# Kernel tuning notes

Measured on AMD Instinct MI355X. Metric: run time of the kernel, lower is better.

The kernel has to match this reference:

```python
import jax, jax.numpy as jnp
import numpy as np

B, D, L, K = 4096, 1280, 16384, 64


def setup_inputs() -> dict:
    key = jax.random.key(0)
    k1, k2, k3, k4, k5 = jax.random.split(key, 5)
    scale_enc = 1.0 / np.sqrt(D)
    scale_dec = 1.0 / np.sqrt(L)
    return {
        "x_BD": jax.random.normal(k1, (B, D), dtype=jnp.float32),
        "pb_D": jax.random.normal(k2, (D,), dtype=jnp.float32) * 0.01,
        "W_enc": jax.random.normal(k3, (D, L), dtype=jnp.float32) * scale_enc,
        "lb_L": jax.random.normal(k4, (L,), dtype=jnp.float32) * 0.01,
        "W_dec": jax.random.normal(k5, (L, D), dtype=jnp.float32) * scale_dec,
    }


def topk_activation(x_BL, k):
    # lax.top_k over last dim, relu the values, scatter back into zeros
    tv_Bk, ti_Bk = jax.lax.top_k(x_BL, k)
    tv_Bk = jax.nn.relu(tv_Bk)
    b_B = jnp.arange(x_BL.shape[0])[:, None]
    return jnp.zeros_like(x_BL).at[b_B, ti_Bk].set(tv_Bk)


def reference(x_BD, pb_D, W_enc, lb_L, W_dec):
    # encode: shift by pre-bias, dense, add latent bias
    xshift_BD = x_BD - pb_D
    zpre_BL = xshift_BD @ W_enc + lb_L          # [B, L]
    # top-k sparse activation
    z_BL = topk_activation(zpre_BL, K)          # [B, L], only K nonzeros per row
    # decode: dense matmul over full L (the kernel-headroom target)
    xhat_BD = z_BL @ W_dec + pb_D               # [B, D]
    return (zpre_BL, z_BL, xhat_BD)
```

## Files before the change

### kernel.cpp

```cpp
#include <hip/hip_runtime.h>
#include <hip/hip_bf16.h>
#include <stdint.h>

#define B_SZ 4096
#define D_SZ 1280
#define L_SZ 16384
#define K_TOP 64
#define C_CAP 192
#define BAND 0.07f

typedef __attribute__((ext_vector_type(8))) short s16x8;
typedef __attribute__((ext_vector_type(4))) float f32x4;

#define GLOAD_LDS16(gp, lp)                                                          \
  __builtin_amdgcn_global_load_lds((const __attribute__((address_space(1))) void*)(gp), \
                                   (__attribute__((address_space(3))) void*)(lp), 16, 0, 0)

static __device__ __forceinline__ unsigned short f2bf(float f) {
  __hip_bfloat16 h = __float2bfloat16(f);
  return *reinterpret_cast<unsigned short*>(&h);
}
static __device__ __forceinline__ float bf2f(unsigned short u) {
  return __uint_as_float((unsigned)u << 16);
}
static __device__ __forceinline__ unsigned mkkey(float f) {
  const unsigned u = __float_as_uint(f);
  return (u & 0x80000000u) ? ~u : (u | 0x80000000u);
}
static __device__ __forceinline__ float unkey(unsigned k) {
  const unsigned u = (k & 0x80000000u) ? (k & 0x7fffffffu) : ~k;
  return __uint_as_float(u);
}

__global__ __launch_bounds__(256) void sae_prep(const float* __restrict__ x,
                                                const float* __restrict__ pb,
                                                const float* __restrict__ We,
                                                const float* __restrict__ Wd,
                                                unsigned short* __restrict__ A,
                                                float* __restrict__ xs,
                                                float* __restrict__ WT,
                                                unsigned short* __restrict__ WbT,
                                                unsigned short* __restrict__ Wdb,
                                                int* __restrict__ bk_cnt) {
  const int b = blockIdx.x, t = threadIdx.x;
  if (b < 5120) {
    __shared__ float tile[64][65];
    const int l0 = (b & 255) * 64, d0 = (b >> 8) * 64;
    const int c = t & 63, rg = t >> 6;
#pragma unroll
    for (int i = 0; i < 16; ++i) {
      const int row = i * 4 + rg;
      tile[row][c] = We[(size_t)(d0 + row) * L_SZ + l0 + c];
    }
    __syncthreads();
#pragma unroll
    for (int i = 0; i < 16; ++i) {
      const int row = i * 4 + rg;
      const float v = tile[c][row];
      const size_t o = (size_t)(l0 + row) * D_SZ + d0 + c;
      WT[o] = v;
      WbT[o] = f2bf(v);
    }
  } else if (b < 5120 + 4096) {
    const int r = b - 5120;
    const float* xr = x + (size_t)r * D_SZ;
    unsigned short* ar = A + (size_t)r * D_SZ;
    float* sr = xs + (size_t)r * D_SZ;
    for (int d = t; d < D_SZ; d += 256) {
      const float v = xr[d] - pb[d];
      ar[d] = f2bf(v);
      sr[d] = v;
    }
  } else if (b < 5120 + 4096 + 2048) {
    const int n4 = L_SZ * D_SZ / 4;
    for (int i = (b - 9216) * 256 + t; i < n4; i += 2048 * 256) {
      const float4 v = ((const float4*)Wd)[i];
      ushort4 o;
      o.x = f2bf(v.x); o.y = f2bf(v.y); o.z = f2bf(v.z); o.w = f2bf(v.w);
      ((ushort4*)Wdb)[i] = o;
    }
  } else {
    bk_cnt[(b - 11264) * 256 + t] = 0;
  }
}

#define SWZ(lin) ((lin) ^ ((((lin) >> 9) & 7) << 4))
#define A_LDS 0
#define B_LDS 65536
#define KBYTES (D_SZ * 2)

#define PH_MID()                                          \
  __builtin_amdgcn_s_barrier();                           \
  asm volatile("s_waitcnt lgkmcnt(0)" ::: "memory");      \
  __builtin_amdgcn_sched_barrier(0);                      \
  __builtin_amdgcn_s_setprio(1)

#define PH_END()                                          \
  __builtin_amdgcn_s_setprio(0);                          \
  __builtin_amdgcn_s_barrier();                           \
  __builtin_amdgcn_sched_barrier(0)

__global__ __launch_bounds__(512, 2) void sae_gemm(const unsigned short* __restrict__ A,
                                                   const unsigned short* __restrict__ WT,
                                                   const float* __restrict__ lb,
                                                   float* __restrict__ zpre) {
  __shared__ short lds[65536];
  char* ldsc = (char*)lds;
  const int t = threadIdx.x, lane = t & 63, w = t >> 6;
  const int wr = w >> 2, wc = w & 3, w2 = w * 2;

  const int bid = blockIdx.x;
  const int xcd = bid & 7, i2 = bid >> 3;
  const int b2 = i2 >> 4, inner = i2 & 15;
  const int mt = (b2 & 3) * 4 + (inner & 3);
  const int nt = xcd * 8 + (b2 >> 2) * 4 + (inner >> 2);
  const int m0 = mt * 256, n0 = nt * 256;

  f32x4 acc[8][4] = {};

  auto STAGE = [&](const unsigned short* op, int rowbase, int ldsop, int buf, int half, int tile) {
#pragma unroll
    for (int s = 0; s < 2; ++s) {
      const int o = (w2 + s) * 1024 + lane * 16;
      const int r = o >> 7;
      const int cb = (o & 127) ^ (((o >> 9) & 7) << 4);
      const char* g = (const char*)op + (size_t)(rowbase + half * 128 + r) * KBYTES +
                      tile * 128 + cb;
      char* l = ldsc + ldsop + buf * 32768 + half * 16384 + (w2 + s) * 1024;
      GLOAD_LDS16(g, l);
    }
  };
  auto LDA = [&](s16x8* af, int buf, int q) {
#pragma unroll
    for (int i = 0; i < 2; ++i)
#pragma unroll
      for (int kk = 0; kk < 2; ++kk) {
        const int r = (q * 2 + i) * 16 + (lane & 15);
        int lin = r * 128 + kk * 64 + ((lane >> 4) * 16);
        lin = SWZ(lin);
        af[i * 2 + kk] = *(const s16x8*)(ldsc + A_LDS + buf * 32768 + wr * 16384 + lin);
      }
  };
  auto LDB = [&](s16x8* bg, int buf) {
#pragma unroll
    for (int j = 0; j < 4; ++j)
#pragma unroll
      for (int kk = 0; kk < 2; ++kk) {
        const int nloc = wc * 64 + j * 16 + (lane & 15);
        const int half = nloc >> 7, r = nloc & 127;
        int lin = r * 128 + kk * 64 + ((lane >> 4) * 16);
        lin = SWZ(lin);
        bg[j * 2 + kk] = *(const s16x8*)(ldsc + B_LDS + buf * 32768 + half * 16384 + lin);
      }
  };
  auto MM = [&](s16x8* af, s16x8* bg, int q) {
#pragma unroll
    for (int i = 0; i < 2; ++i)
#pragma unroll
      for (int j = 0; j < 4; ++j)
#pragma unroll
        for (int kk = 0; kk < 2; ++kk)
          acc[q * 2 + i][j] =
              __builtin_amdgcn_mfma_f32_16x16x32_bf16(af[i * 2 + kk], bg[j * 2 + kk],
                                                      acc[q * 2 + i][j], 0, 0, 0);
  };

  STAGE(WT, n0, B_LDS, 0, 0, 0); STAGE(WT, n0, B_LDS, 0, 1, 0);
  STAGE(A, m0, A_LDS, 0, 0, 0);  STAGE(A, m0, A_LDS, 0, 1, 0);
  STAGE(WT, n0, B_LDS, 1, 0, 1); STAGE(WT, n0, B_LDS, 1, 1, 1);
  asm volatile("s_waitcnt vmcnt(4)" ::: "memory");
  __builtin_amdgcn_s_barrier();
  __builtin_amdgcn_sched_barrier(0);

  const int NI = D_SZ / 128;
  for (int i = 0; i < NI; ++i) {
    const bool last = (i == NI - 1);
    s16x8 af[4], bg[8];
    LDB(bg, 0); LDA(af, 0, 0);
    STAGE(A, m0, A_LDS, 1, 0, 2 * i + 1); STAGE(A, m0, A_LDS, 1, 1, 2 * i + 1);
    PH_MID(); MM(af, bg, 0); PH_END();
    LDA(af, 0, 1);
    if (!last) STAGE(WT, n0, B_LDS, 0, 0, 2 * i + 2);
    PH_MID(); MM(af, bg, 1); PH_END();
    LDA(af, 0, 2);
    if (!last) STAGE(WT, n0, B_LDS, 0, 1, 2 * i + 2);
    PH_MID(); MM(af, bg, 2); PH_END();
    LDA(af, 0, 3);
    PH_MID(); MM(af, bg, 3);
    __builtin_amdgcn_s_setprio(0);
    if (last) { asm volatile("s_waitcnt vmcnt(0)" ::: "memory"); }
    else      { asm volatile("s_waitcnt vmcnt(4)" ::: "memory"); }
    __builtin_amdgcn_s_barrier();
    __builtin_amdgcn_sched_barrier(0);
    LDB(bg, 1); LDA(af, 1, 0);
    if (!last) STAGE(A, m0, A_LDS, 0, 0, 2 * i + 2);
    PH_MID(); MM(af, bg, 0); PH_END();
    LDA(af, 1, 1);
    if (!last) STAGE(A, m0, A_LDS, 0, 1, 2 * i + 2);
    PH_MID(); MM(af, bg, 1); PH_END();
    LDA(af, 1, 2);
    if (!last) STAGE(WT, n0, B_LDS, 1, 0, 2 * i + 3);
    PH_MID(); MM(af, bg, 2); PH_END();
    LDA(af, 1, 3);
    if (!last) STAGE(WT, n0, B_LDS, 1, 1, 2 * i + 3);
    PH_MID(); MM(af, bg, 3);
    __builtin_amdgcn_s_setprio(0);
    asm volatile("s_waitcnt vmcnt(4)" ::: "memory");
    __builtin_amdgcn_s_barrier();
    __builtin_amdgcn_sched_barrier(0);
  }

  const int cl = lane & 15, rg = lane >> 4;
#pragma unroll
  for (int j = 0; j < 4; ++j) {
    const int cc = n0 + wc * 64 + j * 16 + cl;
    const float bias = lb[cc];
#pragma unroll
    for (int i = 0; i < 8; ++i) {
      const size_t base = (size_t)(m0 + wr * 128 + i * 16 + rg * 4) * L_SZ + cc;
#pragma unroll
      for (int tt = 0; tt < 4; ++tt) zpre[base + (size_t)tt * L_SZ] = acc[i][j][tt] + bias;
    }
  }
}

__device__ void radix_pick(unsigned* hist, unsigned* suf, int* sh_b, unsigned* sh_above,
                           int target, int t) {
  if (t == 0) *sh_b = -1;
  unsigned p = hist[4 * t] + hist[4 * t + 1] + hist[4 * t + 2] + hist[4 * t + 3];
  suf[t] = p;
  for (int off = 1; off < 256; off <<= 1) {
    __syncthreads();
    unsigned v = (t + off < 256) ? suf[t + off] : 0u;
    __syncthreads();
    suf[t] += v;
  }
  __syncthreads();
  const unsigned shi = (t + 1 < 256) ? suf[t + 1] : 0u;
  unsigned S = shi;
  int best = -1;
#pragma unroll
  for (int i = 3; i >= 0; --i) {
    S += hist[4 * t + i];
    if (S >= (unsigned)target) { best = 4 * t + i; break; }
  }
  if (best >= 0) atomicMax(sh_b, best);
  __syncthreads();
  const int b = *sh_b;
  if ((b >> 2) == t) {
    unsigned above = shi;
    for (int i = 3; i > (b & 3); --i) above += hist[4 * t + i];
    *sh_above = above;
  }
  __syncthreads();
}

__global__ __launch_bounds__(256) void sae_topc(const float* __restrict__ zpre,
                                                int* __restrict__ bk_cnt,
                                                int* __restrict__ band_lat,
                                                float* __restrict__ band_fval,
                                                int* __restrict__ n_hi,
                                                int* __restrict__ n_band,
                                                int* __restrict__ t_idx,
                                                float* __restrict__ t_val) {
  __shared__ unsigned hist[1024];
  __shared__ unsigned suf[256];
  __shared__ int sh_b0, sh_b1, sh_nhi, sh_nband;
  __shared__ unsigned sh_above;
  const int r = blockIdx.x, t = threadIdx.x;
  const float4* zr4 = (const float4*)(zpre + (size_t)r * L_SZ);

  for (int i = t; i < 1024; i += 256) hist[i] = 0;
  if (t == 0) { sh_nhi = 0; sh_nband = 0; }
  __syncthreads();
  for (int i = t; i < L_SZ / 4; i += 256) {
    const float4 v = zr4[i];
    atomicAdd(&hist[mkkey(v.x) >> 22], 1u);
    atomicAdd(&hist[mkkey(v.y) >> 22], 1u);
    atomicAdd(&hist[mkkey(v.z) >> 22], 1u);
    atomicAdd(&hist[mkkey(v.w) >> 22], 1u);
  }
  __syncthreads();
  radix_pick(hist, suf, &sh_b0, &sh_above, K_TOP, t);
  const int b0 = sh_b0;
  const int target2 = K_TOP - (int)sh_above;
  __syncthreads();
  for (int i = t; i < 1024; i += 256) hist[i] = 0;
  __syncthreads();
  for (int i = t; i < L_SZ / 4; i += 256) {
    const float4 v = zr4[i];
    const float va[4] = {v.x, v.y, v.z, v.w};
#pragma unroll
    for (int q = 0; q < 4; ++q) {
      const unsigned k = mkkey(va[q]);
      if ((int)(k >> 22) == b0) atomicAdd(&hist[(k >> 12) & 1023u], 1u);
    }
  }
  __syncthreads();
  radix_pick(hist, suf, &sh_b1, &sh_above, target2, t);
  const unsigned v64lb_key = (((unsigned)b0 << 10) | (unsigned)sh_b1) << 12;
  const float lo_f = unkey(v64lb_key) - BAND;
  const float hi_f = unkey(v64lb_key + 4095u) + BAND;
  __syncthreads();
  for (int i = t; i < L_SZ / 4; i += 256) {
    const float4 v = zr4[i];
    const float va[4] = {v.x, v.y, v.z, v.w};
#pragma unroll
    for (int q = 0; q < 4; ++q) {
      const float val = va[q];
      if (val >= lo_f) {
        const int l = 4 * i + q;
        if (val > hi_f) {
          const int p = atomicAdd(&sh_nhi, 1);
          if (p < K_TOP) {
            t_idx[(size_t)r * K_TOP + p] = l;
            t_val[(size_t)r * K_TOP + p] = fmaxf(val, 0.f);
          }
        } else {
          const int p = atomicAdd(&sh_nband, 1);
          if (p < C_CAP) {
            band_lat[(r << 8) + p] = l;
            band_fval[(r << 8) + p] = val;
            atomicAdd(&bk_cnt[l], 1);
          }
        }
      }
    }
  }
  __syncthreads();
  if (t == 0) {
    n_hi[r] = sh_nhi < K_TOP ? sh_nhi : K_TOP;
    n_band[r] = sh_nband < C_CAP ? sh_nband : C_CAP;
  }
}

__global__ __launch_bounds__(256) void sae_scan(const int* __restrict__ counts,
                                                int* __restrict__ offsets,
                                                int* __restrict__ cursor) {
  __shared__ int part[256];
  const int t = threadIdx.x;
  int s = 0;
  for (int i = 0; i < 64; ++i) s += counts[t * 64 + i];
  part[t] = s;
  __syncthreads();
  int excl = 0;
  for (int j = 0; j < t; ++j) excl += part[j];
  int run = excl;
  for (int i = 0; i < 64; ++i) {
    const int idx = t * 64 + i;
    offsets[idx] = run;
    cursor[idx] = run;
    run += counts[idx];
  }
}

__global__ __launch_bounds__(192) void sae_bucket_fill(const int* __restrict__ band_lat,
                                                       const int* __restrict__ n_band,
                                                       int* __restrict__ cursor,
                                                       int* __restrict__ entries) {
  const int r = blockIdx.x, t = threadIdx.x;
  if (t < n_band[r]) {
    const int l = band_lat[(r << 8) + t];
    const int pos = atomicAdd(&cursor[l], 1);
    entries[pos] = (r << 8) | t;
  }
}

__global__ __launch_bounds__(256) void sae_refine_lm(const float* __restrict__ xs,
                                                     const float* __restrict__ WT,
                                                     const float* __restrict__ lb,
                                                     const int* __restrict__ counts,
                                                     const int* __restrict__ offsets,
                                                     const int* __restrict__ entries,
                                                     double* __restrict__ band_eval) {
  __shared__ float4 wl[D_SZ / 4];
  const int l = blockIdx.x;
  const int t = threadIdx.x, lane = t & 63, w = t >> 6;
  const int n = counts[l];
  if (n == 0) return;
  const float4* wc = (const float4*)(WT + (size_t)l * D_SZ);
  for (int d = t; d < D_SZ / 4; d += 256) wl[d] = wc[d];
  __syncthreads();
  const int base = offsets[l];
  const double bias = (double)lb[l];
  for (int e = w; e < n; e += 4) {
    const int ent = entries[base + e];
    const int rr = ent >> 8;
    const float4* xr = (const float4*)(xs + (size_t)rr * D_SZ);
    double acc = 0.0;
#pragma unroll
    for (int i = 0; i < 5; ++i) {
      const float4 xv = xr[lane + 64 * i];
      const float4 wv = wl[lane + 64 * i];
      acc += (double)xv.x * (double)wv.x + (double)xv.y * (double)wv.y +
             (double)xv.z * (double)wv.z + (double)xv.w * (double)wv.w;
    }
#pragma unroll
    for (int off = 32; off > 0; off >>= 1) acc += __shfl_down(acc, off);
    if (lane == 0) band_eval[ent] = acc + bias;
  }
}

template <bool WRITE_Z>
__global__ __launch_bounds__(320) void sae_finish(const int* __restrict__ n_hi,
                                                  const int* __restrict__ n_band,
                                                  const int* __restrict__ band_lat,
                                                  const float* __restrict__ band_fval,
                                                  const double* __restrict__ band_eval,
                                                  int* __restrict__ t_idx,
                                                  float* __restrict__ t_val,
                                                  const unsigned short* __restrict__ Wdb,
                                                  const float* __restrict__ pb,
                                                  float* __restrict__ z,
                                                  float* __restrict__ xhat) {
  __shared__ int bl[C_CAP];
  __shared__ float bf[C_CAP];
  __shared__ double be[C_CAP];
  __shared__ int ids[K_TOP];
  __shared__ float vs[K_TOP];
  const int r = blockIdx.x, t = threadIdx.x;
  const int nh = n_hi[r], nb = n_band[r];
  if (t < nb) {
    bl[t] = band_lat[(r << 8) + t];
    bf[t] = band_fval[(r << 8) + t];
    be[t] = band_eval[(r << 8) + t];
  }
  if (t < nh) {
    ids[t] = t_idx[(size_t)r * K_TOP + t];
    vs[t] = t_val[(size_t)r * K_TOP + t];
  }
  __syncthreads();
  const int need = K_TOP - nh;
  if (t < nb) {
    const double ev = be[t];
    const int l = bl[t];
    int rank = 0;
    for (int j = 0; j < nb; ++j) {
      const double e2 = be[j];
      if (e2 > ev || (e2 == ev && bl[j] < l)) ++rank;
    }
    if (rank < need) {
      const float fv = fmaxf(bf[t], 0.f);
      ids[nh + rank] = l;
      vs[nh + rank] = fv;
      t_idx[(size_t)r * K_TOP + nh + rank] = l;
      t_val[(size_t)r * K_TOP + nh + rank] = fv;
    }
  }
  __syncthreads();
  float4 acc = ((const float4*)pb)[t];
#pragma unroll 8
  for (int k = 0; k < K_TOP; ++k) {
    const ushort4 wv = ((const ushort4*)(Wdb + (size_t)ids[k] * D_SZ))[t];
    const float vk = vs[k];
    acc.x += vk * bf2f(wv.x);
    acc.y += vk * bf2f(wv.y);
    acc.z += vk * bf2f(wv.z);
    acc.w += vk * bf2f(wv.w);
  }
  ((float4*)(xhat + (size_t)r * D_SZ))[t] = acc;
  if (WRITE_Z) {
    float4* zr = (float4*)(z + (size_t)r * L_SZ);
    for (int i = t; i < L_SZ / 4; i += 320) zr[i] = make_float4(0.f, 0.f, 0.f, 0.f);
    __syncthreads();
    if (t < K_TOP) z[(size_t)r * L_SZ + ids[t]] = vs[t];
  }
}

__global__ void sae_scatterA(const int* __restrict__ top_idx, const float* __restrict__ top_val,
                             float* __restrict__ z) {
  const int r = blockIdx.x;
  const int t = threadIdx.x;
  const int id = top_idx[(size_t)r * K_TOP + t];
  const float v = top_val[(size_t)r * K_TOP + t];
  z[(size_t)r * L_SZ + id] = v;
}

__global__ __launch_bounds__(256) void sae_scatterB(const int* __restrict__ top_idx,
                                                    const float* __restrict__ top_val,
                                                    float* __restrict__ z) {
  __shared__ int ids[32 * K_TOP];
  __shared__ float vs[32 * K_TOP];
  const int t = threadIdx.x;
  for (int i = t; i < 32 * K_TOP; i += 256) {
    ids[i] = top_idx[(size_t)4064 * K_TOP + i];
    vs[i] = top_val[(size_t)4064 * K_TOP + i];
  }
  __syncthreads();
  float4* zz = (float4*)(z + (size_t)4064 * L_SZ);
  for (int i = t; i < 32 * L_SZ / 4; i += 256) zz[i] = make_float4(0.f, 0.f, 0.f, 0.f);
  __syncthreads();
  for (int i = t; i < 32 * K_TOP; i += 256) {
    const int rr = 4064 + i / K_TOP;
    z[(size_t)rr * L_SZ + ids[i]] = vs[i];
  }
}

extern "C" void kernel_launch(void* const* d_in, const int* in_sizes, int n_in,
                              void* d_out, int out_size, void* d_ws, size_t ws_size,
                              hipStream_t stream) {
  const float* x  = (const float*)d_in[0];
  const float* pb = (const float*)d_in[1];
  const float* We = (const float*)d_in[2];
  const float* lb = (const float*)d_in[3];
  const float* Wd = (const float*)d_in[4];

  float* zpre = (float*)d_out;
  float* z    = zpre + (size_t)B_SZ * L_SZ;
  float* xhat = z + (size_t)B_SZ * L_SZ;

  const bool use_ws = ws_size >= ((size_t)234 << 20);
  char* sb = use_ws ? (char*)d_ws : (char*)z;

  unsigned short* A_bf   = (unsigned short*)(sb);
  unsigned short* WT_bf  = (unsigned short*)(sb + ((size_t)16 << 20));
  float*          WT_f32 = (float*)(sb + ((size_t)64 << 20));
  float*          xs_f32 = (float*)(sb + ((size_t)144 << 20));
  int*            b_lat  = (int*)(sb + ((size_t)164 << 20));
  float*          b_fval = (float*)(sb + ((size_t)168 << 20));
  double*         b_eval = (double*)(sb + ((size_t)172 << 20));
  int*            bk_cnt = (int*)(sb + ((size_t)180 << 20));
  int*            bk_off = (int*)(sb + ((size_t)181 << 20));
  int*            bk_cur = (int*)(sb + ((size_t)182 << 20));
  int*            bk_ent = (int*)(sb + ((size_t)184 << 20));
  unsigned short* Wd_bf  = (unsigned short*)(sb + ((size_t)188 << 20));
  int*            nhi_g  = (int*)(sb + ((size_t)228 << 20));
  int*            nbd_g  = (int*)(sb + ((size_t)229 << 20));
  int*   t_idx = use_ws ? (int*)(sb + ((size_t)230 << 20))
                        : (int*)((char*)z + ((size_t)254 << 20));
  float* t_val = use_ws ? (float*)(sb + ((size_t)232 << 20))
                        : (float*)((char*)z + ((size_t)255 << 20));

  sae_prep<<<11328, 256, 0, stream>>>(x, pb, We, Wd, A_bf, xs_f32, WT_f32, WT_bf, Wd_bf, bk_cnt);
  sae_gemm<<<1024, 512, 0, stream>>>(A_bf, WT_bf, lb, zpre);
  sae_topc<<<B_SZ, 256, 0, stream>>>(zpre, bk_cnt, b_lat, b_fval, nhi_g, nbd_g, t_idx, t_val);
  sae_scan<<<1, 256, 0, stream>>>(bk_cnt, bk_off, bk_cur);
  sae_bucket_fill<<<B_SZ, 192, 0, stream>>>(b_lat, nbd_g, bk_cur, bk_ent);
  sae_refine_lm<<<L_SZ, 256, 0, stream>>>(xs_f32, WT_f32, lb, bk_cnt, bk_off, bk_ent, b_eval);
  if (use_ws) {
    sae_finish<true><<<B_SZ, 320, 0, stream>>>(nhi_g, nbd_g, b_lat, b_fval, b_eval, t_idx, t_val,
                                               Wd_bf, pb, z, xhat);
  } else {
    sae_finish<false><<<B_SZ, 320, 0, stream>>>(nhi_g, nbd_g, b_lat, b_fval, b_eval, t_idx, t_val,
                                                Wd_bf, pb, z, xhat);
    hipMemsetAsync(z, 0, (size_t)4064 * L_SZ * sizeof(float), stream);
    sae_scatterA<<<4064, K_TOP, 0, stream>>>(t_idx, t_val, z);
    sae_scatterB<<<1, 256, 0, stream>>>(t_idx, t_val, z);
  }
}
```

Baseline: 657.6 us.

## Fuse top-k selection, band refinement and decode into one per-row kernel

When workspace is available, the per-row top-k radix selection, FP64 refinement of borderline candidates, decode matvec and z write are merged into a single 512-thread kernel. The row is cached in LDS (64 KB) so it is read from global memory once. The band refinement is now done per row by dotting against the gathered WT rows, replacing the bucketed, latent-major pass. This removes four launches and the intermediate global buffers, but the large LDS footprint limits occupancy and each row re-reads WT rows instead of sharing them across rows per latent.

```diff
diff --git a/kernel.cpp b/kernel.cpp
--- a/kernel.cpp
+++ b/kernel.cpp
@@ -255,6 +255,161 @@
   __syncthreads();
 }
 
+__device__ void radix_pick512(unsigned* hist, unsigned* suf, int* sh_b, unsigned* sh_above,
+                              int target, int t) {
+  if (t == 0) *sh_b = -1;
+  if (t < 256) suf[t] = hist[4 * t] + hist[4 * t + 1] + hist[4 * t + 2] + hist[4 * t + 3];
+  for (int off = 1; off < 256; off <<= 1) {
+    __syncthreads();
+    unsigned v = (t < 256 && t + off < 256) ? suf[t + off] : 0u;
+    __syncthreads();
+    if (t < 256) suf[t] += v;
+  }
+  __syncthreads();
+  if (t < 256) {
+    const unsigned shi = (t + 1 < 256) ? suf[t + 1] : 0u;
+    unsigned S = shi;
+    int best = -1;
+#pragma unroll
+    for (int i = 3; i >= 0; --i) {
+      S += hist[4 * t + i];
+      if (S >= (unsigned)target) { best = 4 * t + i; break; }
+    }
+    if (best >= 0) atomicMax(sh_b, best);
+  }
+  __syncthreads();
+  const int b = *sh_b;
+  if (t < 256 && (b >> 2) == t) {
+    unsigned above = (t + 1 < 256) ? suf[t + 1] : 0u;
+    for (int i = 3; i > (b & 3); --i) above += hist[4 * t + i];
+    *sh_above = above;
+  }
+  __syncthreads();
+}
+
+__global__ __launch_bounds__(512) void sae_mega(const float* __restrict__ zpre,
+                                                const float* __restrict__ xs,
+                                                const float* __restrict__ WT,
+                                                const float* __restrict__ lb,
+                                                const unsigned short* __restrict__ Wdb,
+                                                const float* __restrict__ pb,
+                                                float* __restrict__ z,
+                                                float* __restrict__ xhat) {
+  __shared__ float row[L_SZ];
+  __shared__ unsigned hist[1024];
+  __shared__ unsigned suf[256];
+  __shared__ int sh_b0, sh_b1, sh_nhi, sh_nband;
+  __shared__ unsigned sh_above;
+  __shared__ int bl[C_CAP];
+  __shared__ float bfv[C_CAP];
+  __shared__ double be[C_CAP];
+  __shared__ int ids[K_TOP];
+  __shared__ float vs[K_TOP];
+
+  const int r = blockIdx.x, t = threadIdx.x, lane = t & 63, w = t >> 6;
+  const float4* zr4 = (const float4*)(zpre + (size_t)r * L_SZ);
+
+  float4 xc[5];
+  {
+    const float4* xr4 = (const float4*)(xs + (size_t)r * D_SZ);
+#pragma unroll
+    for (int i = 0; i < 5; ++i) xc[i] = xr4[lane + 64 * i];
+  }
+
+  for (int i = t; i < 1024; i += 512) hist[i] = 0;
+  if (t == 0) { sh_nhi = 0; sh_nband = 0; }
+  __syncthreads();
+  for (int i = t; i < L_SZ / 4; i += 512) {
+    const float4 v = zr4[i];
+    ((float4*)row)[i] = v;
+    atomicAdd(&hist[mkkey(v.x) >> 22], 1u);
+    atomicAdd(&hist[mkkey(v.y) >> 22], 1u);
+    atomicAdd(&hist[mkkey(v.z) >> 22], 1u);
+    atomicAdd(&hist[mkkey(v.w) >> 22], 1u);
+  }
+  __syncthreads();
+  radix_pick512(hist, suf, &sh_b0, &sh_above, K_TOP, t);
+  const int b0 = sh_b0;
+  const int target2 = K_TOP - (int)sh_above;
+  __syncthreads();
+  for (int i = t; i < 1024; i += 512) hist[i] = 0;
+  __syncthreads();
+  for (int i = t; i < L_SZ; i += 512) {
+    const unsigned k = mkkey(row[i]);
+    if ((int)(k >> 22) == b0) atomicAdd(&hist[(k >> 12) & 1023u], 1u);
+  }
+  __syncthreads();
+  radix_pick512(hist, suf, &sh_b1, &sh_above, target2, t);
+  const unsigned v64lb_key = (((unsigned)b0 << 10) | (unsigned)sh_b1) << 12;
+  const float lo_f = unkey(v64lb_key) - BAND;
+  const float hi_f = unkey(v64lb_key + 4095u) + BAND;
+  __syncthreads();
+  for (int i = t; i < L_SZ; i += 512) {
+    const float val = row[i];
+    if (val >= lo_f) {
+      if (val > hi_f) {
+        const int p = atomicAdd(&sh_nhi, 1);
+        if (p < K_TOP) { ids[p] = i; vs[p] = fmaxf(val, 0.f); }
+      } else {
+        const int p = atomicAdd(&sh_nband, 1);
+        if (p < C_CAP) { bl[p] = i; bfv[p] = val; }
+      }
+    }
+  }
+  __syncthreads();
+  const int nh = sh_nhi < K_TOP ? sh_nhi : K_TOP;
+  const int nb = sh_nband < C_CAP ? sh_nband : C_CAP;
+  for (int e = w; e < nb; e += 8) {
+    const int l = bl[e];
+    const float4* wr4 = (const float4*)(WT + (size_t)l * D_SZ);
+    double acc = 0.0;
+#pragma unroll
+    for (int i = 0; i < 5; ++i) {
+      const float4 wv = wr4[lane + 64 * i];
+      acc += (double)xc[i].x * (double)wv.x + (double)xc[i].y * (double)wv.y +
+             (double)xc[i].z * (double)wv.z + (double)xc[i].w * (double)wv.w;
+    }
+#pragma unroll
+    for (int off = 32; off > 0; off >>= 1) acc += __shfl_down(acc, off);
+    if (lane == 0) be[e] = acc + (double)lb[l];
+  }
+  __syncthreads();
+  const int need = K_TOP - nh;
+  if (t < nb) {
+    const double ev = be[t];
+    const int l = bl[t];
+    int rank = 0;
+    for (int j = 0; j < nb; ++j) {
+      const double e2 = be[j];
+      if (e2 > ev || (e2 == ev && bl[j] < l)) ++rank;
+    }
+    if (rank < need) {
+      ids[nh + rank] = l;
+      vs[nh + rank] = fmaxf(bfv[t], 0.f);
+    }
+  }
+  __syncthreads();
+  if (t < 320) {
+    float4 acc = ((const float4*)pb)[t];
+#pragma unroll 8
+    for (int k = 0; k < K_TOP; ++k) {
+      const ushort4 wv = ((const ushort4*)(Wdb + (size_t)ids[k] * D_SZ))[t];
+      const float vk = vs[k];
+      acc.x += vk * bf2f(wv.x);
+      acc.y += vk * bf2f(wv.y);
+      acc.z += vk * bf2f(wv.z);
+      acc.w += vk * bf2f(wv.w);
+    }
+    ((float4*)(xhat + (size_t)r * D_SZ))[t] = acc;
+  } else {
+    const int tz = t - 320;
+    float4* zr = (float4*)(z + (size_t)r * L_SZ);
+    for (int i = tz; i < L_SZ / 4; i += 192) zr[i] = make_float4(0.f, 0.f, 0.f, 0.f);
+  }
+  __syncthreads();
+  if (t < K_TOP) z[(size_t)r * L_SZ + ids[t]] = vs[t];
+}
+
 __global__ __launch_bounds__(256) void sae_topc(const float* __restrict__ zpre,
                                                 int* __restrict__ bk_cnt,
                                                 int* __restrict__ band_lat,
@@ -401,18 +556,16 @@
   }
 }
 
-template <bool WRITE_Z>
-__global__ __launch_bounds__(320) void sae_finish(const int* __restrict__ n_hi,
-                                                  const int* __restrict__ n_band,
-                                                  const int* __restrict__ band_lat,
-                                                  const float* __restrict__ band_fval,
-                                                  const double* __restrict__ band_eval,
-                                                  int* __restrict__ t_idx,
-                                                  float* __restrict__ t_val,
-                                                  const unsigned short* __restrict__ Wdb,
-                                                  const float* __restrict__ pb,
-                                                  float* __restrict__ z,
-                                                  float* __restrict__ xhat) {
+__global__ __launch_bounds__(320) void sae_finish_nz(const int* __restrict__ n_hi,
+                                                     const int* __restrict__ n_band,
+                                                     const int* __restrict__ band_lat,
+                                                     const float* __restrict__ band_fval,
+                                                     const double* __restrict__ band_eval,
+                                                     int* __restrict__ t_idx,
+                                                     float* __restrict__ t_val,
+                                                     const unsigned short* __restrict__ Wdb,
+                                                     const float* __restrict__ pb,
+                                                     float* __restrict__ xhat) {
   __shared__ int bl[C_CAP];
   __shared__ float bf[C_CAP];
   __shared__ double be[C_CAP];
@@ -459,12 +612,6 @@
     acc.w += vk * bf2f(wv.w);
   }
   ((float4*)(xhat + (size_t)r * D_SZ))[t] = acc;
-  if (WRITE_Z) {
-    float4* zr = (float4*)(z + (size_t)r * L_SZ);
-    for (int i = t; i < L_SZ / 4; i += 320) zr[i] = make_float4(0.f, 0.f, 0.f, 0.f);
-    __syncthreads();
-    if (t < K_TOP) z[(size_t)r * L_SZ + ids[t]] = vs[t];
-  }
 }
 
 __global__ void sae_scatterA(const int* __restrict__ top_idx, const float* __restrict__ top_val,
@@ -533,16 +680,15 @@
 
   sae_prep<<<11328, 256, 0, stream>>>(x, pb, We, Wd, A_bf, xs_f32, WT_f32, WT_bf, Wd_bf, bk_cnt);
   sae_gemm<<<1024, 512, 0, stream>>>(A_bf, WT_bf, lb, zpre);
-  sae_topc<<<B_SZ, 256, 0, stream>>>(zpre, bk_cnt, b_lat, b_fval, nhi_g, nbd_g, t_idx, t_val);
-  sae_scan<<<1, 256, 0, stream>>>(bk_cnt, bk_off, bk_cur);
-  sae_bucket_fill<<<B_SZ, 192, 0, stream>>>(b_lat, nbd_g, bk_cur, bk_ent);
-  sae_refine_lm<<<L_SZ, 256, 0, stream>>>(xs_f32, WT_f32, lb, bk_cnt, bk_off, bk_ent, b_eval);
   if (use_ws) {
-    sae_finish<true><<<B_SZ, 320, 0, stream>>>(nhi_g, nbd_g, b_lat, b_fval, b_eval, t_idx, t_val,
-                                               Wd_bf, pb, z, xhat);
+    sae_mega<<<B_SZ, 512, 0, stream>>>(zpre, xs_f32, WT_f32, lb, Wd_bf, pb, z, xhat);
   } else {
-    sae_finish<false><<<B_SZ, 320, 0, stream>>>(nhi_g, nbd_g, b_lat, b_fval, b_eval, t_idx, t_val,
-                                                Wd_bf, pb, z, xhat);
+    sae_topc<<<B_SZ, 256, 0, stream>>>(zpre, bk_cnt, b_lat, b_fval, nhi_g, nbd_g, t_idx, t_val);
+    sae_scan<<<1, 256, 0, stream>>>(bk_cnt, bk_off, bk_cur);
+    sae_bucket_fill<<<B_SZ, 192, 0, stream>>>(b_lat, nbd_g, bk_cur, bk_ent);
+    sae_refine_lm<<<L_SZ, 256, 0, stream>>>(xs_f32, WT_f32, lb, bk_cnt, bk_off, bk_ent, b_eval);
+    sae_finish_nz<<<B_SZ, 320, 0, stream>>>(nhi_g, nbd_g, b_lat, b_fval, b_eval, t_idx, t_val,
+                                            Wd_bf, pb, xhat);
     hipMemsetAsync(z, 0, (size_t)4064 * L_SZ * sizeof(float), stream);
     sae_scatterA<<<4064, K_TOP, 0, stream>>>(t_idx, t_val, z);
     sae_scatterB<<<1, 256, 0, stream>>>(t_idx, t_val, z);
```

New measurement: 673.4 us. 2.4% more time.
